# Performance work log

Hardware: AMD Instinct MI355X
Metric: run time of the kernel (lower is better)

Reference implementation:

```python
import jax, jax.numpy as jnp
import numpy as np

B, H, D, RD = 32, 16, 256, 64          # batch, heads, head_dim, rotary_dim
NE, NI = 4096, 16384                   # n_embd, n_inner
SLOTS, KVL = 32768, 1024               # paged cache slots, per-batch kv length
EPS = 1e-5


def setup_inputs() -> dict:
    key = jax.random.key(0)
    ks = jax.random.split(key, 12)
    s = 0.02
    return {
        "hidden_states": jax.random.normal(ks[0], (B, 1, NE), jnp.float32),
        "key_cache": jax.random.normal(ks[1], (SLOTS, H, D), jnp.float32),
        "value_cache": jax.random.normal(ks[2], (SLOTS, H, D), jnp.float32),
        "ln_w": jnp.ones((NE,), jnp.float32),
        "ln_b": jnp.zeros((NE,), jnp.float32),
        "wq": jax.random.normal(ks[3], (NE, NE), jnp.float32) * s,
        "wk": jax.random.normal(ks[4], (NE, NE), jnp.float32) * s,
        "wv": jax.random.normal(ks[5], (NE, NE), jnp.float32) * s,
        "wo": jax.random.normal(ks[6], (NE, NE), jnp.float32) * s,
        "fc_in_w": jax.random.normal(ks[7], (NE, NI), jnp.float32) * s,
        "fc_in_b": jnp.zeros((NI,), jnp.float32),
        "fc_out_w": jax.random.normal(ks[8], (NI, NE), jnp.float32) * s,
        "fc_out_b": jnp.zeros((NE,), jnp.float32),
        "attention_mask": jnp.zeros((B, 1, 1, KVL), jnp.float32),
        "new_key_location": jnp.arange(B, dtype=jnp.int32),
        "new_value_location": jnp.arange(B, dtype=jnp.int32),
        "past_valid_key_decode_indices": jax.random.randint(ks[9], (B, KVL), 0, SLOTS, jnp.int32),
        "past_valid_value_decode_indices": jax.random.randint(ks[10], (B, KVL), 0, SLOTS, jnp.int32),
        "position_ids": jax.random.randint(ks[11], (B, 1), 0, KVL, jnp.int32),
    }


def _rope(x, position_ids):
    # GPT-J rotate-every-two rotary on first RD dims. x: [B, S, H, D]
    half = RD // 2
    inv_freq = 1.0 / (10000.0 ** (jnp.arange(0, RD, 2, dtype=jnp.float32) / RD))  # [half]
    ang = position_ids.astype(jnp.float32)[..., None] * inv_freq  # [B, S, half]
    sin = jnp.sin(ang)[:, :, None, :]  # [B, S, 1, half]
    cos = jnp.cos(ang)[:, :, None, :]
    xr, xp = x[..., :RD], x[..., RD:]
    x1, x2 = xr[..., 0::2], xr[..., 1::2]
    o1 = x1 * cos - x2 * sin
    o2 = x2 * cos + x1 * sin
    rot = jnp.stack([o1, o2], axis=-1).reshape(xr.shape)
    return jnp.concatenate([rot, xp], axis=-1)


def reference(hidden_states, key_cache, value_cache, ln_w, ln_b, wq, wk, wv, wo,
              fc_in_w, fc_in_b, fc_out_w, fc_out_b, attention_mask,
              new_key_location, new_value_location,
              past_valid_key_decode_indices, past_valid_value_decode_indices,
              position_ids):
    residual = hidden_states[:, -1:, :]                       # [B, 1, NE]
    mu = jnp.mean(hidden_states, axis=-1, keepdims=True)
    var = jnp.mean(jnp.square(hidden_states - mu), axis=-1, keepdims=True)
    h = (hidden_states - mu) * jax.lax.rsqrt(var + EPS) * ln_w + ln_b

    q = (h @ wq).reshape(B, 1, H, D)
    k = (h @ wk).reshape(B, 1, H, D)
    v = (h @ wv).reshape(B, 1, H, D)
    q = _rope(q, position_ids)
    k = _rope(k, position_ids)

    # paged KV update: scatter new token, gather valid slots per batch
    kc = key_cache.at[new_key_location].set(k[:, 0])          # [SLOTS, H, D]
    vc = value_cache.at[new_value_location].set(v[:, 0])
    K = kc[past_valid_key_decode_indices]                     # [B, KVL, H, D]
    V = vc[past_valid_value_decode_indices]                   # [B, KVL, H, D]

    scale = jnp.asarray(np.sqrt(D), jnp.float32)
    scores = jnp.einsum("bqhd,blhd->bhql", q, K) / scale + attention_mask
    p = jax.nn.softmax(scores, axis=-1)                       # [B, H, 1, KVL]
    ctx = jnp.einsum("bhql,blhd->bqhd", p, V).reshape(B, 1, NE)
    attn_out = ctx @ wo

    m = jax.nn.gelu(h[:, -1:, :] @ fc_in_w + fc_in_b, approximate=True)
    mlp_out = m @ fc_out_w + fc_out_b

    return attn_out + mlp_out + residual
```

## Files before the change

### kernel.cpp

```cpp
#include <hip/hip_runtime.h>
#include <math.h>

#define BB 32
#define HH 16
#define DD 256
#define RDIM 64
#define NEMB 4096
#define NINT 16384
#define NSLOTS 32768
#define KVLEN 1024
#define LNEPS 1e-5f
#define NCH 16
#define CH 64

__global__ __launch_bounds__(256) void ln_kernel(const float* __restrict__ x,
    const float* __restrict__ lw, const float* __restrict__ lb,
    float* __restrict__ hT)
{
    int b = blockIdx.x;
    int t = threadIdx.x;
    const float* row = x + (size_t)b * NEMB;
    float4 v[4];
    float sum = 0.f, sq = 0.f;
#pragma unroll
    for (int j = 0; j < 4; ++j) {
        v[j] = *(const float4*)(row + t * 4 + j * 1024);
        sum += v[j].x + v[j].y + v[j].z + v[j].w;
        sq += v[j].x * v[j].x + v[j].y * v[j].y + v[j].z * v[j].z + v[j].w * v[j].w;
    }
    __shared__ float s1[4], s2[4];
#pragma unroll
    for (int o = 32; o > 0; o >>= 1) {
        sum += __shfl_xor(sum, o, 64);
        sq += __shfl_xor(sq, o, 64);
    }
    int wave = t >> 6, lane = t & 63;
    if (lane == 0) { s1[wave] = sum; s2[wave] = sq; }
    __syncthreads();
    sum = s1[0] + s1[1] + s1[2] + s1[3];
    sq = s2[0] + s2[1] + s2[2] + s2[3];
    float mu = sum / NEMB;
    float var = sq / NEMB - mu * mu;
    float rstd = rsqrtf(var + LNEPS);
#pragma unroll
    for (int j = 0; j < 4; ++j) {
        int n = t * 4 + j * 1024;
        float4 wv = *(const float4*)(lw + n);
        float4 bv = *(const float4*)(lb + n);
        hT[(size_t)(n + 0) * BB + b] = (v[j].x - mu) * rstd * wv.x + bv.x;
        hT[(size_t)(n + 1) * BB + b] = (v[j].y - mu) * rstd * wv.y + bv.y;
        hT[(size_t)(n + 2) * BB + b] = (v[j].z - mu) * rstd * wv.z + bv.z;
        hT[(size_t)(n + 3) * BB + b] = (v[j].w - mu) * rstd * wv.w + bv.w;
    }
}

__device__ __forceinline__ void gemm_body(const float* __restrict__ AT,
    const float* __restrict__ W, float* __restrict__ P,
    int N, int kChunk, int x, int s)
{
    int n = (x * 256 + threadIdx.x) * 2;
    size_t k0 = (size_t)s * kChunk;
    float2 acc[32];
#pragma unroll
    for (int mi = 0; mi < 32; ++mi) acc[mi] = make_float2(0.f, 0.f);
    const float* w = W + k0 * N + n;
    const float* a = AT + k0 * 32;
#pragma unroll 4
    for (int kk = 0; kk < kChunk; ++kk) {
        float2 wv = *(const float2*)w;
#pragma unroll
        for (int mi = 0; mi < 32; ++mi) {
            float am = a[mi];
            acc[mi].x = fmaf(am, wv.x, acc[mi].x);
            acc[mi].y = fmaf(am, wv.y, acc[mi].y);
        }
        w += N;
        a += 32;
    }
    float* p = P + ((size_t)s * 32) * N + n;
#pragma unroll
    for (int mi = 0; mi < 32; ++mi)
        *(float2*)(p + (size_t)mi * N) = acc[mi];
}

__device__ __forceinline__ void gemm_body64(const float* __restrict__ AT,
    const float* __restrict__ W, float* __restrict__ P,
    int N, int kChunk, int x, int s)
{
    int n = (x * 64 + threadIdx.x) * 2;
    size_t k0 = (size_t)s * kChunk;
    float2 acc[32];
#pragma unroll
    for (int mi = 0; mi < 32; ++mi) acc[mi] = make_float2(0.f, 0.f);
    const float* w = W + k0 * N + n;
    const float* a = AT + k0 * 32;
#pragma unroll 4
    for (int kk = 0; kk < kChunk; ++kk) {
        float2 wv = *(const float2*)w;
#pragma unroll
        for (int mi = 0; mi < 32; ++mi) {
            float am = a[mi];
            acc[mi].x = fmaf(am, wv.x, acc[mi].x);
            acc[mi].y = fmaf(am, wv.y, acc[mi].y);
        }
        w += N;
        a += 32;
    }
    float* p = P + ((size_t)s * 32) * N + n;
#pragma unroll
    for (int mi = 0; mi < 32; ++mi)
        *(float2*)(p + (size_t)mi * N) = acc[mi];
}

__global__ __launch_bounds__(256) void phase2_kernel(const float* __restrict__ hT,
    const float* __restrict__ wq, const float* __restrict__ wk, const float* __restrict__ wv,
    float* __restrict__ Pq, const float* __restrict__ fciw, float* __restrict__ P1)
{
    int id = blockIdx.x;
    if (id < 768) {
        int w = id >> 8;
        const float* W = (w == 0) ? wq : (w == 1) ? wk : wv;
        float* Pz = Pq + (size_t)w * ((size_t)32 * 32 * NEMB);
        gemm_body(hT, W, Pz, NEMB, 128, id & 7, (id >> 3) & 31);
    } else {
        id -= 768;
        gemm_body(hT, fciw, P1, NINT, 256, id & 31, id >> 5);
    }
}

__device__ inline float gelu_tanh(float x)
{
    float x3 = x * x * x;
    return 0.5f * x * (1.f + tanhf(0.7978845608028654f * (x + 0.044715f * x3)));
}

__global__ __launch_bounds__(256) void phase3_kernel(const float* __restrict__ Pq,
    float* __restrict__ q, float* __restrict__ k, float* __restrict__ v,
    const int* __restrict__ pos,
    const float* __restrict__ P1, const float* __restrict__ fcib, float* __restrict__ mT)
{
    int id = blockIdx.x, t = threadIdx.x;
    if (id < 768) {
        int w = id >> 8;
        int m = (id >> 3) & 31;
        int n0 = ((id & 7) * 256 + t) * 2;
        const float* p = Pq + (size_t)w * ((size_t)32 * 32 * NEMB) + (size_t)m * NEMB + n0;
        float sx = 0.f, sy = 0.f;
#pragma unroll 4
        for (int i = 0; i < 32; ++i) {
            float2 u = *(const float2*)p;
            sx += u.x; sy += u.y;
            p += (size_t)32 * NEMB;
        }
        int d = n0 & (DD - 1);
        if (w < 2 && d < RDIM) {
            int i = d >> 1;
            float fr = exp2f((float)i * (-13.287712379549449f / 32.f));
            float ang = (float)pos[m] * fr;
            float sn, cs;
            sincosf(ang, &sn, &cs);
            float x1 = sx, x2 = sy;
            sx = x1 * cs - x2 * sn;
            sy = x2 * cs + x1 * sn;
        }
        float* o = (w == 0) ? q : (w == 1) ? k : v;
        *(float2*)(o + (size_t)m * NEMB + n0) = make_float2(sx, sy);
    } else {
        int j = id - 768;
        int m = j >> 6;
        int n = (j & 63) * 256 + t;
        const float* p = P1 + (size_t)m * NINT + n;
        float s = 0.f;
#pragma unroll 4
        for (int i = 0; i < 16; ++i) { s += *p; p += (size_t)32 * NINT; }
        mT[(size_t)n * 32 + m] = gelu_tanh(s + fcib[n]);
    }
}

__global__ __launch_bounds__(64) void phase4_kernel(const float* __restrict__ q,
    const float* __restrict__ knew, const float* __restrict__ vnew,
    const float* __restrict__ kcache, const float* __restrict__ vcache,
    const int* __restrict__ kidx, const int* __restrict__ vidx,
    const int* __restrict__ nkl, const int* __restrict__ nvl,
    const float* __restrict__ mask,
    float* __restrict__ pm, float* __restrict__ pl, float* __restrict__ pctx,
    const float* __restrict__ mT, const float* __restrict__ fcow, float* __restrict__ P2)
{
    int id = blockIdx.x;
    int t = threadIdx.x;
    if (id < 2048) {
        gemm_body64(mT, fcow, P2, NEMB, 256, id & 31, id >> 5);
        return;
    }
    id -= 2048;
    int bh = id >> 4, c = id & 15;
    int b = bh >> 4, h = bh & 15;

    __shared__ const float* kparr[CH];
    __shared__ const float* vparr[CH];
    __shared__ float sc[CH];

    {
        int ks = kidx[b * KVLEN + c * CH + t];
        int vs = vidx[b * KVLEN + c * CH + t];
        const float* kbase = kcache + (size_t)ks * NEMB;
        const float* vbase = vcache + (size_t)vs * NEMB;
#pragma unroll
        for (int j = 0; j < BB; ++j) {
            if (nkl[j] == ks) kbase = knew + (size_t)j * NEMB;
            if (nvl[j] == vs) vbase = vnew + (size_t)j * NEMB;
        }
        kparr[t] = kbase + (size_t)h * DD;
        vparr[t] = vbase + (size_t)h * DD;
    }
    __syncthreads();

    int u = t & 15, g = t >> 4;
    float4 qf[4];
#pragma unroll
    for (int j = 0; j < 4; ++j) qf[j] = *(const float4*)(q + (size_t)b * NEMB + (size_t)h * DD + u * 4 + j * 64);

#pragma unroll 4
    for (int it = 0; it < 16; ++it) {
        int l = it * 4 + g;
        const float* kr = kparr[l];
        float d = 0.f;
#pragma unroll
        for (int j = 0; j < 4; ++j) {
            float4 kf = *(const float4*)(kr + u * 4 + j * 64);
            d = fmaf(kf.x, qf[j].x, fmaf(kf.y, qf[j].y, fmaf(kf.z, qf[j].z, fmaf(kf.w, qf[j].w, d))));
        }
        d += __shfl_xor(d, 8, 64);
        d += __shfl_xor(d, 4, 64);
        d += __shfl_xor(d, 2, 64);
        d += __shfl_xor(d, 1, 64);
        if (u == 0) sc[l] = d * 0.0625f + mask[b * KVLEN + c * CH + l];
    }
    __syncthreads();

    float sv = sc[t];
    float mx = sv;
#pragma unroll
    for (int o = 32; o > 0; o >>= 1) mx = fmaxf(mx, __shfl_xor(mx, o, 64));
    float e = expf(sv - mx);
    float sm = e;
#pragma unroll
    for (int o = 32; o > 0; o >>= 1) sm += __shfl_xor(sm, o, 64);

    float4 a4 = make_float4(0.f, 0.f, 0.f, 0.f);
#pragma unroll 8
    for (int l = 0; l < CH; ++l) {
        const float* vr = vparr[l];
        float4 vf = *(const float4*)(vr + t * 4);
        float pw = __shfl(e, l, 64);
        a4.x = fmaf(pw, vf.x, a4.x);
        a4.y = fmaf(pw, vf.y, a4.y);
        a4.z = fmaf(pw, vf.z, a4.z);
        a4.w = fmaf(pw, vf.w, a4.w);
    }

    int pi = bh * NCH + c;
    *(float4*)(pctx + (size_t)pi * DD + t * 4) = a4;
    if (t == 0) { pm[pi] = mx; pl[pi] = sm; }
}

__global__ __launch_bounds__(256) void attn_comb_kernel(const float* __restrict__ pm,
    const float* __restrict__ pl, const float* __restrict__ pctx,
    float* __restrict__ ctxT)
{
    int bh = blockIdx.x;
    int b = bh >> 4, h = bh & 15;
    int t = threadIdx.x;
    float M = -INFINITY;
#pragma unroll
    for (int c = 0; c < NCH; ++c) M = fmaxf(M, pm[bh * NCH + c]);
    float L = 0.f, acc = 0.f;
#pragma unroll
    for (int c = 0; c < NCH; ++c) {
        float wv = expf(pm[bh * NCH + c] - M);
        L += pl[bh * NCH + c] * wv;
        acc += pctx[((size_t)bh * NCH + c) * DD + t] * wv;
    }
    ctxT[((size_t)h * DD + t) * BB + b] = acc / L;
}

__global__ __launch_bounds__(256) void phase6_kernel(const float* __restrict__ ctxT,
    const float* __restrict__ wo, float* __restrict__ P0,
    const float* __restrict__ P2, const float* __restrict__ fcob,
    const float* __restrict__ resid, float* __restrict__ mlp_tmp)
{
    int id = blockIdx.x, t = threadIdx.x;
    if (id < 512) {
        gemm_body(ctxT, wo, P0, NEMB, 64, id & 7, id >> 3);
    } else {
        int j = id - 512;
        int m = j >> 4;
        int n = (j & 15) * 256 + t;
        const float* p = P2 + (size_t)m * NEMB + n;
        float s = 0.f;
#pragma unroll 4
        for (int i = 0; i < 64; ++i) { s += *p; p += (size_t)32 * NEMB; }
        mlp_tmp[(size_t)m * NEMB + n] = s + fcob[n] + resid[(size_t)m * NEMB + n];
    }
}

__global__ __launch_bounds__(256) void phase7_kernel(const float* __restrict__ P0,
    const float* __restrict__ mlp_tmp, float* __restrict__ out)
{
    int n = blockIdx.x * 256 + threadIdx.x;
    int m = blockIdx.y;
    const float* p = P0 + (size_t)m * NEMB + n;
    float s = 0.f;
#pragma unroll 4
    for (int i = 0; i < 64; ++i) { s += *p; p += (size_t)32 * NEMB; }
    out[(size_t)m * NEMB + n] = s + mlp_tmp[(size_t)m * NEMB + n];
}

extern "C" void kernel_launch(void* const* d_in, const int* in_sizes, int n_in,
                              void* d_out, int out_size, void* d_ws, size_t ws_size,
                              hipStream_t stream)
{
    (void)in_sizes; (void)n_in; (void)out_size; (void)ws_size;
    const float* hs      = (const float*)d_in[0];
    const float* kcache  = (const float*)d_in[1];
    const float* vcache  = (const float*)d_in[2];
    const float* ln_w    = (const float*)d_in[3];
    const float* ln_b    = (const float*)d_in[4];
    const float* wq      = (const float*)d_in[5];
    const float* wk      = (const float*)d_in[6];
    const float* wv      = (const float*)d_in[7];
    const float* wo      = (const float*)d_in[8];
    const float* fc_in_w = (const float*)d_in[9];
    const float* fc_in_b = (const float*)d_in[10];
    const float* fc_out_w= (const float*)d_in[11];
    const float* fc_out_b= (const float*)d_in[12];
    const float* mask    = (const float*)d_in[13];
    const int* nkl       = (const int*)d_in[14];
    const int* nvl       = (const int*)d_in[15];
    const int* kidx      = (const int*)d_in[16];
    const int* vidx      = (const int*)d_in[17];
    const int* pos       = (const int*)d_in[18];
    float* out = (float*)d_out;

    char* ws = (char*)d_ws;
    float* hT      = (float*)ws; ws += (size_t)NEMB * BB * 4;
    float* qb      = (float*)ws; ws += (size_t)BB * NEMB * 4;
    float* kb      = (float*)ws; ws += (size_t)BB * NEMB * 4;
    float* vb      = (float*)ws; ws += (size_t)BB * NEMB * 4;
    float* ctxT    = (float*)ws; ws += (size_t)NEMB * BB * 4;
    float* mlp_tmp = (float*)ws; ws += (size_t)BB * NEMB * 4;
    float* mT      = (float*)ws; ws += (size_t)NINT * BB * 4;
    float* pm      = (float*)ws; ws += (size_t)BB * HH * NCH * 4;
    float* pl      = (float*)ws; ws += (size_t)BB * HH * NCH * 4;
    float* pctx    = (float*)ws; ws += (size_t)BB * HH * NCH * DD * 4;
    float* Pq      = (float*)ws; ws += (size_t)3 * 32 * 32 * NEMB * 4;
    float* P0      = (float*)ws; ws += (size_t)64 * 32 * NEMB * 4;
    float* P1      = (float*)ws; ws += (size_t)16 * 32 * NINT * 4;
    float* P2      = (float*)ws;

    ln_kernel<<<BB, 256, 0, stream>>>(hs, ln_w, ln_b, hT);

    phase2_kernel<<<1280, 256, 0, stream>>>(hT, wq, wk, wv, Pq, fc_in_w, P1);

    phase3_kernel<<<2816, 256, 0, stream>>>(Pq, qb, kb, vb, pos, P1, fc_in_b, mT);

    phase4_kernel<<<10240, 64, 0, stream>>>(qb, kb, vb, kcache, vcache,
                                            kidx, vidx, nkl, nvl, mask,
                                            pm, pl, pctx, mT, fc_out_w, P2);

    attn_comb_kernel<<<BB * HH, 256, 0, stream>>>(pm, pl, pctx, ctxT);

    phase6_kernel<<<1024, 256, 0, stream>>>(ctxT, wo, P0, P2, fc_out_b, hs, mlp_tmp);

    phase7_kernel<<<dim3(16, 32), 256, 0, stream>>>(P0, mlp_tmp, out);
}
```

Baseline: 448.0 us.

## Double-buffer K/V rows into LDS via async global_load_lds and halve QKV split-K

The attention chunk kernel now stages gathered K and V rows into a double-buffered LDS buffer with direct global-to-LDS loads, prefetching two batches of eight rows ahead and waiting with explicit vmcnt counters. The previous direct per-row global loads had limited memory-level parallelism. The QKV projection split-K factor is also halved (K chunk 256 instead of 128), which reduces partial-sum traffic and the reduction loop in phase3 but leaves fewer blocks. Each score now needs a full 64-lane shuffle reduction per row, and correctness depends on the hand-written waitcnt ordering.

```diff
diff --git a/kernel.cpp b/kernel.cpp
--- a/kernel.cpp
+++ b/kernel.cpp
@@ -12,6 +12,7 @@
 #define LNEPS 1e-5f
 #define NCH 16
 #define CH 64
+#define BATCH 8
 
 __global__ __launch_bounds__(256) void ln_kernel(const float* __restrict__ x,
     const float* __restrict__ lw, const float* __restrict__ lb,
@@ -117,13 +118,13 @@
     float* __restrict__ Pq, const float* __restrict__ fciw, float* __restrict__ P1)
 {
     int id = blockIdx.x;
-    if (id < 768) {
-        int w = id >> 8;
+    if (id < 384) {
+        int w = id >> 7;
         const float* W = (w == 0) ? wq : (w == 1) ? wk : wv;
-        float* Pz = Pq + (size_t)w * ((size_t)32 * 32 * NEMB);
-        gemm_body(hT, W, Pz, NEMB, 128, id & 7, (id >> 3) & 31);
+        float* Pz = Pq + (size_t)w * ((size_t)16 * 32 * NEMB);
+        gemm_body(hT, W, Pz, NEMB, 256, id & 7, (id >> 3) & 15);
     } else {
-        id -= 768;
+        id -= 384;
         gemm_body(hT, fciw, P1, NINT, 256, id & 31, id >> 5);
     }
 }
@@ -144,10 +145,10 @@
         int w = id >> 8;
         int m = (id >> 3) & 31;
         int n0 = ((id & 7) * 256 + t) * 2;
-        const float* p = Pq + (size_t)w * ((size_t)32 * 32 * NEMB) + (size_t)m * NEMB + n0;
+        const float* p = Pq + (size_t)w * ((size_t)16 * 32 * NEMB) + (size_t)m * NEMB + n0;
         float sx = 0.f, sy = 0.f;
 #pragma unroll 4
-        for (int i = 0; i < 32; ++i) {
+        for (int i = 0; i < 16; ++i) {
             float2 u = *(const float2*)p;
             sx += u.x; sy += u.y;
             p += (size_t)32 * NEMB;
@@ -177,6 +178,19 @@
     }
 }
 
+template<int N>
+__device__ __forceinline__ void waitcnt_vm()
+{
+    asm volatile("s_waitcnt vmcnt(%0)" :: "i"(N) : "memory");
+}
+
+__device__ __forceinline__ void gload_lds16(const float* src, float* dst)
+{
+    __builtin_amdgcn_global_load_lds(
+        (const __attribute__((address_space(1))) void*)src,
+        (__attribute__((address_space(3))) void*)dst, 16, 0, 0);
+}
+
 __global__ __launch_bounds__(64) void phase4_kernel(const float* __restrict__ q,
     const float* __restrict__ knew, const float* __restrict__ vnew,
     const float* __restrict__ kcache, const float* __restrict__ vcache,
@@ -196,9 +210,9 @@
     int bh = id >> 4, c = id & 15;
     int b = bh >> 4, h = bh & 15;
 
+    __shared__ float kvbuf[2][BATCH * DD];
     __shared__ const float* kparr[CH];
     __shared__ const float* vparr[CH];
-    __shared__ float sc[CH];
 
     {
         int ks = kidx[b * KVLEN + c * CH + t];
@@ -213,32 +227,53 @@
         kparr[t] = kbase + (size_t)h * DD;
         vparr[t] = vbase + (size_t)h * DD;
     }
-    __syncthreads();
-
-    int u = t & 15, g = t >> 4;
-    float4 qf[4];
-#pragma unroll
-    for (int j = 0; j < 4; ++j) qf[j] = *(const float4*)(q + (size_t)b * NEMB + (size_t)h * DD + u * 4 + j * 64);
-
-#pragma unroll 4
-    for (int it = 0; it < 16; ++it) {
-        int l = it * 4 + g;
-        const float* kr = kparr[l];
-        float d = 0.f;
-#pragma unroll
-        for (int j = 0; j < 4; ++j) {
-            float4 kf = *(const float4*)(kr + u * 4 + j * 64);
-            d = fmaf(kf.x, qf[j].x, fmaf(kf.y, qf[j].y, fmaf(kf.z, qf[j].z, fmaf(kf.w, qf[j].w, d))));
-        }
-        d += __shfl_xor(d, 8, 64);
-        d += __shfl_xor(d, 4, 64);
-        d += __shfl_xor(d, 2, 64);
-        d += __shfl_xor(d, 1, 64);
-        if (u == 0) sc[l] = d * 0.0625f + mask[b * KVLEN + c * CH + l];
-    }
-    __syncthreads();
-
-    float sv = sc[t];
+
+    float maskreg = mask[b * KVLEN + c * CH + t];
+    float4 qf = *(const float4*)(q + (size_t)b * NEMB + (size_t)h * DD + t * 4);
+    waitcnt_vm<0>();
+    __builtin_amdgcn_sched_barrier(0);
+
+#pragma unroll
+    for (int r = 0; r < BATCH; ++r)
+        gload_lds16(kparr[r] + t * 4, &kvbuf[0][r * DD]);
+#pragma unroll
+    for (int r = 0; r < BATCH; ++r)
+        gload_lds16(kparr[BATCH + r] + t * 4, &kvbuf[1][r * DD]);
+
+    float sv = 0.f;
+#pragma unroll
+    for (int i = 0; i < 8; ++i) {
+        if (i < 7) waitcnt_vm<BATCH>(); else waitcnt_vm<0>();
+        __builtin_amdgcn_sched_barrier(0);
+        const float* kb_ = &kvbuf[i & 1][0];
+#pragma unroll
+        for (int r = 0; r < BATCH; ++r) {
+            float4 kf = *(const float4*)(kb_ + r * DD + t * 4);
+            float d = fmaf(kf.x, qf.x, fmaf(kf.y, qf.y, fmaf(kf.z, qf.z, kf.w * qf.w)));
+            d += __shfl_xor(d, 32, 64);
+            d += __shfl_xor(d, 16, 64);
+            d += __shfl_xor(d, 8, 64);
+            d += __shfl_xor(d, 4, 64);
+            d += __shfl_xor(d, 2, 64);
+            d += __shfl_xor(d, 1, 64);
+            int row = i * BATCH + r;
+            if (t == row) sv = d * 0.0625f + maskreg;
+        }
+        __builtin_amdgcn_sched_barrier(0);
+        if (i + 2 < 8) {
+#pragma unroll
+            for (int r = 0; r < BATCH; ++r)
+                gload_lds16(kparr[(i + 2) * BATCH + r] + t * 4, &kvbuf[i & 1][r * DD]);
+        }
+    }
+
+#pragma unroll
+    for (int r = 0; r < BATCH; ++r)
+        gload_lds16(vparr[r] + t * 4, &kvbuf[0][r * DD]);
+#pragma unroll
+    for (int r = 0; r < BATCH; ++r)
+        gload_lds16(vparr[BATCH + r] + t * 4, &kvbuf[1][r * DD]);
+
     float mx = sv;
 #pragma unroll
     for (int o = 32; o > 0; o >>= 1) mx = fmaxf(mx, __shfl_xor(mx, o, 64));
@@ -248,15 +283,26 @@
     for (int o = 32; o > 0; o >>= 1) sm += __shfl_xor(sm, o, 64);
 
     float4 a4 = make_float4(0.f, 0.f, 0.f, 0.f);
-#pragma unroll 8
-    for (int l = 0; l < CH; ++l) {
-        const float* vr = vparr[l];
-        float4 vf = *(const float4*)(vr + t * 4);
-        float pw = __shfl(e, l, 64);
-        a4.x = fmaf(pw, vf.x, a4.x);
-        a4.y = fmaf(pw, vf.y, a4.y);
-        a4.z = fmaf(pw, vf.z, a4.z);
-        a4.w = fmaf(pw, vf.w, a4.w);
+#pragma unroll
+    for (int i = 0; i < 8; ++i) {
+        if (i < 7) waitcnt_vm<BATCH>(); else waitcnt_vm<0>();
+        __builtin_amdgcn_sched_barrier(0);
+        const float* vb_ = &kvbuf[i & 1][0];
+#pragma unroll
+        for (int r = 0; r < BATCH; ++r) {
+            float4 vf = *(const float4*)(vb_ + r * DD + t * 4);
+            float pw = __shfl(e, i * BATCH + r, 64);
+            a4.x = fmaf(pw, vf.x, a4.x);
+            a4.y = fmaf(pw, vf.y, a4.y);
+            a4.z = fmaf(pw, vf.z, a4.z);
+            a4.w = fmaf(pw, vf.w, a4.w);
+        }
+        __builtin_amdgcn_sched_barrier(0);
+        if (i + 2 < 8) {
+#pragma unroll
+            for (int r = 0; r < BATCH; ++r)
+                gload_lds16(vparr[(i + 2) * BATCH + r] + t * 4, &kvbuf[i & 1][r * DD]);
+        }
     }
 
     int pi = bh * NCH + c;
@@ -353,14 +399,14 @@
     float* pm      = (float*)ws; ws += (size_t)BB * HH * NCH * 4;
     float* pl      = (float*)ws; ws += (size_t)BB * HH * NCH * 4;
     float* pctx    = (float*)ws; ws += (size_t)BB * HH * NCH * DD * 4;
-    float* Pq      = (float*)ws; ws += (size_t)3 * 32 * 32 * NEMB * 4;
+    float* Pq      = (float*)ws; ws += (size_t)3 * 16 * 32 * NEMB * 4;
     float* P0      = (float*)ws; ws += (size_t)64 * 32 * NEMB * 4;
     float* P1      = (float*)ws; ws += (size_t)16 * 32 * NINT * 4;
     float* P2      = (float*)ws;
 
     ln_kernel<<<BB, 256, 0, stream>>>(hs, ln_w, ln_b, hT);
 
-    phase2_kernel<<<1280, 256, 0, stream>>>(hT, wq, wk, wv, Pq, fc_in_w, P1);
+    phase2_kernel<<<896, 256, 0, stream>>>(hT, wq, wk, wv, Pq, fc_in_w, P1);
 
     phase3_kernel<<<2816, 256, 0, stream>>>(Pq, qb, kb, vb, pos, P1, fc_in_b, mT);
 
```

Result: slower. 458.9 us (+2.4%).

## Deduplicate paged K reads via per-slot inverted index before attention

Applied to the files above, without the earlier changes.

Builds a per-slot inverted index of key-decode positions with atomics inside phase2. A new scores kernel then reads each referenced K cache row once and computes its dot products for every (batch, position) that uses it. Phase4 now only does softmax from the precomputed scores plus the V accumulation, and the chunk combine becomes a plain sum because normalisation moves into phase4. This cuts redundant K gather traffic. In exchange it adds a 32768-block launch, a scores buffer, and redundant 1024-wide softmax reductions in every chunk block. It also silently drops entries if any slot is referenced more than CAP=20 times.

```diff
diff --git a/kernel.cpp b/kernel.cpp
--- a/kernel.cpp
+++ b/kernel.cpp
@@ -12,13 +12,19 @@
 #define LNEPS 1e-5f
 #define NCH 16
 #define CH 64
-
-__global__ __launch_bounds__(256) void ln_kernel(const float* __restrict__ x,
+#define CAP 20
+
+__global__ __launch_bounds__(256) void ln_init_kernel(const float* __restrict__ x,
     const float* __restrict__ lw, const float* __restrict__ lb,
-    float* __restrict__ hT)
-{
+    float* __restrict__ hT, int* __restrict__ cnt)
+{
+    int t = threadIdx.x;
+    if (blockIdx.x >= BB) {
+        int i = (blockIdx.x - BB) * 256 + t;
+        if (i < NSLOTS) cnt[i] = 0;
+        return;
+    }
     int b = blockIdx.x;
-    int t = threadIdx.x;
     const float* row = x + (size_t)b * NEMB;
     float4 v[4];
     float sum = 0.f, sq = 0.f;
@@ -114,7 +120,8 @@
 
 __global__ __launch_bounds__(256) void phase2_kernel(const float* __restrict__ hT,
     const float* __restrict__ wq, const float* __restrict__ wk, const float* __restrict__ wv,
-    float* __restrict__ Pq, const float* __restrict__ fciw, float* __restrict__ P1)
+    float* __restrict__ Pq, const float* __restrict__ fciw, float* __restrict__ P1,
+    const int* __restrict__ kidx, int* __restrict__ cnt, int* __restrict__ ent)
 {
     int id = blockIdx.x;
     if (id < 768) {
@@ -122,9 +129,14 @@
         const float* W = (w == 0) ? wq : (w == 1) ? wk : wv;
         float* Pz = Pq + (size_t)w * ((size_t)32 * 32 * NEMB);
         gemm_body(hT, W, Pz, NEMB, 128, id & 7, (id >> 3) & 31);
-    } else {
+    } else if (id < 1280) {
         id -= 768;
         gemm_body(hT, fciw, P1, NINT, 256, id & 31, id >> 5);
+    } else {
+        int i = (id - 1280) * 256 + threadIdx.x;
+        int s = kidx[i];
+        int pos = atomicAdd(&cnt[s], 1);
+        if (pos < CAP) ent[s * CAP + pos] = i;
     }
 }
 
@@ -177,13 +189,47 @@
     }
 }
 
-__global__ __launch_bounds__(64) void phase4_kernel(const float* __restrict__ q,
-    const float* __restrict__ knew, const float* __restrict__ vnew,
-    const float* __restrict__ kcache, const float* __restrict__ vcache,
-    const int* __restrict__ kidx, const int* __restrict__ vidx,
-    const int* __restrict__ nkl, const int* __restrict__ nvl,
-    const float* __restrict__ mask,
-    float* __restrict__ pm, float* __restrict__ pl, float* __restrict__ pctx,
+__global__ __launch_bounds__(256) void scores_kernel(const float* __restrict__ q,
+    const float* __restrict__ knew, const float* __restrict__ kcache,
+    const int* __restrict__ nkl, const int* __restrict__ cnt, const int* __restrict__ ent,
+    const float* __restrict__ mask, float* __restrict__ scores)
+{
+    int s = blockIdx.x;
+    int n = cnt[s];
+    if (n == 0) return;
+    if (n > CAP) n = CAP;
+    int t = threadIdx.x;
+    int h = t >> 4, u = t & 15;
+    const float* row = kcache + (size_t)s * NEMB;
+#pragma unroll
+    for (int j = 0; j < BB; ++j)
+        if (nkl[j] == s) row = knew + (size_t)j * NEMB;
+    float4 kf[4];
+    const float* rp = row + h * DD + u * 16;
+#pragma unroll
+    for (int j = 0; j < 4; ++j) kf[j] = *(const float4*)(rp + j * 4);
+    for (int e = 0; e < n; ++e) {
+        int bl = ent[s * CAP + e];
+        int b = bl >> 10, l = bl & 1023;
+        const float* qp = q + (size_t)b * NEMB + h * DD + u * 16;
+        float d = 0.f;
+#pragma unroll
+        for (int j = 0; j < 4; ++j) {
+            float4 qf = *(const float4*)(qp + j * 4);
+            d = fmaf(kf[j].x, qf.x, fmaf(kf[j].y, qf.y, fmaf(kf[j].z, qf.z, fmaf(kf[j].w, qf.w, d))));
+        }
+        d += __shfl_xor(d, 8, 64);
+        d += __shfl_xor(d, 4, 64);
+        d += __shfl_xor(d, 2, 64);
+        d += __shfl_xor(d, 1, 64);
+        if (u == 0) scores[((size_t)b * HH + h) * KVLEN + l] = d * 0.0625f + mask[b * KVLEN + l];
+    }
+}
+
+__global__ __launch_bounds__(64) void phase4_kernel(
+    const float* __restrict__ vnew, const float* __restrict__ vcache,
+    const int* __restrict__ vidx, const int* __restrict__ nvl,
+    const float* __restrict__ scores, float* __restrict__ pctx,
     const float* __restrict__ mT, const float* __restrict__ fcow, float* __restrict__ P2)
 {
     int id = blockIdx.x;
@@ -196,56 +242,37 @@
     int bh = id >> 4, c = id & 15;
     int b = bh >> 4, h = bh & 15;
 
-    __shared__ const float* kparr[CH];
     __shared__ const float* vparr[CH];
-    __shared__ float sc[CH];
 
     {
-        int ks = kidx[b * KVLEN + c * CH + t];
         int vs = vidx[b * KVLEN + c * CH + t];
-        const float* kbase = kcache + (size_t)ks * NEMB;
         const float* vbase = vcache + (size_t)vs * NEMB;
 #pragma unroll
-        for (int j = 0; j < BB; ++j) {
-            if (nkl[j] == ks) kbase = knew + (size_t)j * NEMB;
+        for (int j = 0; j < BB; ++j)
             if (nvl[j] == vs) vbase = vnew + (size_t)j * NEMB;
-        }
-        kparr[t] = kbase + (size_t)h * DD;
         vparr[t] = vbase + (size_t)h * DD;
     }
+
+    const float* sr = scores + (size_t)bh * KVLEN;
+    float4 s4[4];
+    const float* sp = sr + t * 16;
+#pragma unroll
+    for (int j = 0; j < 4; ++j) s4[j] = *(const float4*)(sp + j * 4);
+    float mx = -INFINITY;
+#pragma unroll
+    for (int j = 0; j < 4; ++j)
+        mx = fmaxf(mx, fmaxf(fmaxf(s4[j].x, s4[j].y), fmaxf(s4[j].z, s4[j].w)));
+#pragma unroll
+    for (int o = 32; o > 0; o >>= 1) mx = fmaxf(mx, __shfl_xor(mx, o, 64));
+    float sm = 0.f;
+#pragma unroll
+    for (int j = 0; j < 4; ++j)
+        sm += expf(s4[j].x - mx) + expf(s4[j].y - mx) + expf(s4[j].z - mx) + expf(s4[j].w - mx);
+#pragma unroll
+    for (int o = 32; o > 0; o >>= 1) sm += __shfl_xor(sm, o, 64);
+    float inv = 1.f / sm;
+    float e = expf(sr[c * CH + t] - mx) * inv;
     __syncthreads();
-
-    int u = t & 15, g = t >> 4;
-    float4 qf[4];
-#pragma unroll
-    for (int j = 0; j < 4; ++j) qf[j] = *(const float4*)(q + (size_t)b * NEMB + (size_t)h * DD + u * 4 + j * 64);
-
-#pragma unroll 4
-    for (int it = 0; it < 16; ++it) {
-        int l = it * 4 + g;
-        const float* kr = kparr[l];
-        float d = 0.f;
-#pragma unroll
-        for (int j = 0; j < 4; ++j) {
-            float4 kf = *(const float4*)(kr + u * 4 + j * 64);
-            d = fmaf(kf.x, qf[j].x, fmaf(kf.y, qf[j].y, fmaf(kf.z, qf[j].z, fmaf(kf.w, qf[j].w, d))));
-        }
-        d += __shfl_xor(d, 8, 64);
-        d += __shfl_xor(d, 4, 64);
-        d += __shfl_xor(d, 2, 64);
-        d += __shfl_xor(d, 1, 64);
-        if (u == 0) sc[l] = d * 0.0625f + mask[b * KVLEN + c * CH + l];
-    }
-    __syncthreads();
-
-    float sv = sc[t];
-    float mx = sv;
-#pragma unroll
-    for (int o = 32; o > 0; o >>= 1) mx = fmaxf(mx, __shfl_xor(mx, o, 64));
-    float e = expf(sv - mx);
-    float sm = e;
-#pragma unroll
-    for (int o = 32; o > 0; o >>= 1) sm += __shfl_xor(sm, o, 64);
 
     float4 a4 = make_float4(0.f, 0.f, 0.f, 0.f);
 #pragma unroll 8
@@ -261,27 +288,19 @@
 
     int pi = bh * NCH + c;
     *(float4*)(pctx + (size_t)pi * DD + t * 4) = a4;
-    if (t == 0) { pm[pi] = mx; pl[pi] = sm; }
-}
-
-__global__ __launch_bounds__(256) void attn_comb_kernel(const float* __restrict__ pm,
-    const float* __restrict__ pl, const float* __restrict__ pctx,
+}
+
+__global__ __launch_bounds__(256) void attn_comb_kernel(const float* __restrict__ pctx,
     float* __restrict__ ctxT)
 {
     int bh = blockIdx.x;
     int b = bh >> 4, h = bh & 15;
     int t = threadIdx.x;
-    float M = -INFINITY;
-#pragma unroll
-    for (int c = 0; c < NCH; ++c) M = fmaxf(M, pm[bh * NCH + c]);
-    float L = 0.f, acc = 0.f;
-#pragma unroll
-    for (int c = 0; c < NCH; ++c) {
-        float wv = expf(pm[bh * NCH + c] - M);
-        L += pl[bh * NCH + c] * wv;
-        acc += pctx[((size_t)bh * NCH + c) * DD + t] * wv;
-    }
-    ctxT[((size_t)h * DD + t) * BB + b] = acc / L;
+    float acc = 0.f;
+#pragma unroll
+    for (int c = 0; c < NCH; ++c)
+        acc += pctx[((size_t)bh * NCH + c) * DD + t];
+    ctxT[((size_t)h * DD + t) * BB + b] = acc;
 }
 
 __global__ __launch_bounds__(256) void phase6_kernel(const float* __restrict__ ctxT,
@@ -350,25 +369,29 @@
     float* ctxT    = (float*)ws; ws += (size_t)NEMB * BB * 4;
     float* mlp_tmp = (float*)ws; ws += (size_t)BB * NEMB * 4;
     float* mT      = (float*)ws; ws += (size_t)NINT * BB * 4;
-    float* pm      = (float*)ws; ws += (size_t)BB * HH * NCH * 4;
-    float* pl      = (float*)ws; ws += (size_t)BB * HH * NCH * 4;
+    int*   cnt     = (int*)ws;   ws += (size_t)NSLOTS * 4;
+    int*   ent     = (int*)ws;   ws += (size_t)NSLOTS * CAP * 4;
+    float* scores  = (float*)ws; ws += (size_t)BB * HH * KVLEN * 4;
     float* pctx    = (float*)ws; ws += (size_t)BB * HH * NCH * DD * 4;
     float* Pq      = (float*)ws; ws += (size_t)3 * 32 * 32 * NEMB * 4;
     float* P0      = (float*)ws; ws += (size_t)64 * 32 * NEMB * 4;
     float* P1      = (float*)ws; ws += (size_t)16 * 32 * NINT * 4;
     float* P2      = (float*)ws;
 
-    ln_kernel<<<BB, 256, 0, stream>>>(hs, ln_w, ln_b, hT);
-
-    phase2_kernel<<<1280, 256, 0, stream>>>(hT, wq, wk, wv, Pq, fc_in_w, P1);
+    ln_init_kernel<<<160, 256, 0, stream>>>(hs, ln_w, ln_b, hT, cnt);
+
+    phase2_kernel<<<1408, 256, 0, stream>>>(hT, wq, wk, wv, Pq, fc_in_w, P1,
+                                            kidx, cnt, ent);
 
     phase3_kernel<<<2816, 256, 0, stream>>>(Pq, qb, kb, vb, pos, P1, fc_in_b, mT);
 
-    phase4_kernel<<<10240, 64, 0, stream>>>(qb, kb, vb, kcache, vcache,
-                                            kidx, vidx, nkl, nvl, mask,
-                                            pm, pl, pctx, mT, fc_out_w, P2);
-
-    attn_comb_kernel<<<BB * HH, 256, 0, stream>>>(pm, pl, pctx, ctxT);
+    scores_kernel<<<NSLOTS, 256, 0, stream>>>(qb, kb, kcache, nkl, cnt, ent,
+                                              mask, scores);
+
+    phase4_kernel<<<10240, 64, 0, stream>>>(vb, vcache, vidx, nvl,
+                                            scores, pctx, mT, fc_out_w, P2);
+
+    attn_comb_kernel<<<BB * HH, 256, 0, stream>>>(pctx, ctxT);
 
     phase6_kernel<<<1024, 256, 0, stream>>>(ctxT, wo, P0, P2, fc_out_b, hs, mlp_tmp);
 
```

Result: slower. 474.3 us (+5.9%).
